# Optimization experiments

Measured on AMD Instinct MI355X. Metric: run time of the kernel, lower is better.

The kernel has to match this reference:

```python
import jax, jax.numpy as jnp
import numpy as np

N = 100000       # nodes
E = 3200000      # directed edges (before self-loops)
F_IN = 256       # num_node_features
HID = 8          # hidden per head (conv1)
HEADS = 8        # conv1 heads
C_OUT = 1        # conv2 out channels / heads=1


def setup_inputs() -> dict:
    key = jax.random.key(0)
    ks = jax.random.split(key, 10)
    s = 0.1
    return {
        "x": jax.random.normal(ks[0], (N, F_IN), jnp.float32),
        "edge_index": jax.random.randint(ks[1], (2, E), 0, N, dtype=jnp.int32),
        "W1": jax.random.normal(ks[2], (F_IN, HEADS * HID), jnp.float32) * s,
        "att_src1": jax.random.normal(ks[3], (HEADS, HID), jnp.float32) * s,
        "att_dst1": jax.random.normal(ks[4], (HEADS, HID), jnp.float32) * s,
        "b1": jnp.zeros((HEADS * HID,), jnp.float32),
        "W2": jax.random.normal(ks[5], (HEADS * HID, C_OUT), jnp.float32) * s,
        "att_src2": jax.random.normal(ks[6], (1, C_OUT), jnp.float32) * s,
        "att_dst2": jax.random.normal(ks[7], (1, C_OUT), jnp.float32) * s,
        "b2": jnp.zeros((C_OUT,), jnp.float32),
    }


def gat_conv(x, W, att_src, att_dst, bias, src, dst, heads, out_ch, concat):
    # PyG GATConv (eval mode): h = x @ W per head; alpha over incoming edges of dst.
    h = (x @ W).reshape(-1, heads, out_ch)                 # [N, H, C]
    a_s = jnp.einsum('nhc,hc->nh', h, att_src)             # source term
    a_d = jnp.einsum('nhc,hc->nh', h, att_dst)             # target term
    e = jax.nn.leaky_relu(a_s[src] + a_d[dst], 0.2)        # [Etot, H]
    # segment softmax over edges grouped by target node
    m = jax.ops.segment_max(e, dst, num_segments=N)
    ex = jnp.exp(e - m[dst])
    denom = jax.ops.segment_sum(ex, dst, num_segments=N)
    alpha = ex / (denom[dst] + 1e-16)                      # [Etot, H]
    out = jax.ops.segment_sum(h[src] * alpha[..., None], dst, num_segments=N)
    out = out.reshape(-1, heads * out_ch) if concat else out.mean(axis=1)
    return out + bias


def reference(x, edge_index, W1, att_src1, att_dst1, b1, W2, att_src2, att_dst2, b2):
    # add self-loops (GATConv default add_self_loops=True)
    loop = jnp.arange(N, dtype=edge_index.dtype)
    src = jnp.concatenate([edge_index[0], loop])
    dst = jnp.concatenate([edge_index[1], loop])
    # dropout layers are identity in eval mode
    h = gat_conv(x, W1, att_src1, att_dst1, b1, src, dst, HEADS, HID, True)
    h = jax.nn.elu(h)
    out = gat_conv(h, W2, att_src2, att_dst2, b2, src, dst, 1, C_OUT, False)
    return jax.nn.sigmoid(out)
```

## Files before the change

kernel.cpp:

```cpp
#include <hip/hip_runtime.h>
#include <math.h>

#define FIN 256
#define C1  64
#define NH  8
#define HID 8
#define MAXBUK 512
#define CAPLOG 14
#define SC_CHUNK 8192
#define EPT (SC_CHUNK / 512)

typedef unsigned short ushort_t;
typedef unsigned int uint_t;
typedef __attribute__((ext_vector_type(8))) short short8;
typedef __attribute__((ext_vector_type(4))) float f32x4;

__device__ __forceinline__ ushort_t f2bf(float f) {
    uint_t u = __float_as_uint(f);
    u += 0x7fffu + ((u >> 16) & 1u);
    return (ushort_t)(u >> 16);
}
__device__ __forceinline__ uint_t packbf2(float lo, float hi) {
    return (uint_t)f2bf(lo) | ((uint_t)f2bf(hi) << 16);
}
__device__ __forceinline__ float bf_lo(uint_t w) { return __uint_as_float(w << 16); }
__device__ __forceinline__ float bf_hi(uint_t w) { return __uint_as_float(w & 0xffff0000u); }

__global__ void k_prep(const float* __restrict__ W, ushort_t* __restrict__ Wtg,
                       int* __restrict__ bkt_cnt) {
    int tid = blockIdx.x * 256 + threadIdx.x;
    if (tid < MAXBUK) bkt_cnt[tid] = 0;
    int c = tid >> 8;
    int k = tid & 255;
    Wtg[c * 256 + k] = f2bf(W[k * C1 + c]);
}

__global__ __launch_bounds__(512) void k_bscatter(const int* __restrict__ ei, int E, int N,
                                                  int NBUK, int* __restrict__ bkt_cnt,
                                                  uint_t* __restrict__ ebuf) {
    __shared__ int hist[MAXBUK];
    __shared__ int loff[MAXBUK];
    __shared__ int delta[MAXBUK];
    __shared__ int ssum[MAXBUK];
    __shared__ uint_t vals[SC_CHUNK];
    __shared__ ushort_t buks[SC_CHUNK];

    const int t = threadIdx.x;
    hist[t] = 0;
    __syncthreads();

    const int Etot = E + N;
    const int base0 = blockIdx.x * SC_CHUNK;
    const int lim = min(base0 + SC_CHUNK, Etot);
    const int cnt = lim - base0;

    uint_t myval[EPT];
    int myb[EPT];
#pragma unroll
    for (int i = 0; i < EPT; ++i) {
        int e = base0 + t + i * 512;
        if (e < lim) {
            int s, d;
            if (e < E) { s = ei[e]; d = ei[E + e]; } else { s = e - E; d = s; }
            myval[i] = ((uint_t)s << 8) | (uint_t)(d & 255);
            myb[i] = d >> 8;
            atomicAdd(&hist[myb[i]], 1);
        } else myb[i] = -1;
    }
    __syncthreads();

    int v = hist[t];
    ssum[t] = v;
    __syncthreads();
    for (int o = 1; o < 512; o <<= 1) {
        int add = (t >= o) ? ssum[t - o] : 0;
        __syncthreads();
        ssum[t] += add;
        __syncthreads();
    }
    loff[t] = ssum[t] - v;
    __syncthreads();

    if (t < NBUK) {
        int c = hist[t];
        if (c) delta[t] = (t << CAPLOG) + atomicAdd(&bkt_cnt[t], c) - loff[t];
    }
    __syncthreads();

#pragma unroll
    for (int i = 0; i < EPT; ++i) {
        if (myb[i] >= 0) {
            int pos = atomicAdd(&loff[myb[i]], 1);
            vals[pos] = myval[i];
            buks[pos] = (ushort_t)myb[i];
        }
    }
    __syncthreads();

    for (int i = t; i < cnt; i += 512)
        ebuf[delta[buks[i]] + i] = vals[i];
}

__global__ __launch_bounds__(512) void k_bucket_csr(const uint_t* __restrict__ ebuf,
                                                    const int* __restrict__ bkt_cnt, int N,
                                                    int* __restrict__ deg, int* __restrict__ off,
                                                    int* __restrict__ csr) {
    __shared__ int degw[8 * 256];
    __shared__ int scan[256];
    __shared__ int curl[256];
    int b = blockIdx.x;
    int t = threadIdx.x;
    int wv = t >> 6;
    int beg = b << CAPLOG;
    int end = beg + bkt_cnt[b];
    for (int i = t; i < 8 * 256; i += 512) degw[i] = 0;
    __syncthreads();
    for (int j = beg + t; j < end; j += 512) {
        uint_t v = ebuf[j];
        atomicAdd(&degw[(wv << 8) + (v & 255u)], 1);
    }
    __syncthreads();
    int v = 0;
    if (t < 256) {
#pragma unroll
        for (int w = 0; w < 8; ++w) v += degw[(w << 8) + t];
        scan[t] = v;
    }
    __syncthreads();
    for (int o = 1; o < 256; o <<= 1) {
        int a = (t < 256 && t >= o) ? scan[t - o] : 0;
        __syncthreads();
        if (t < 256) scan[t] += a;
        __syncthreads();
    }
    if (t < 256) {
        int gpos = beg + scan[t] - v;
        int node = (b << 8) + t;
        if (node < N) { off[node] = gpos; deg[node] = v; }
        curl[t] = gpos;
    }
    __syncthreads();
    for (int j = beg + t; j < end; j += 512) {
        uint_t p = ebuf[j];
        int pos = atomicAdd(&curl[p & 255u], 1);
        csr[pos] = (int)(p >> 8);
    }
}

__global__ __launch_bounds__(256) void k_gemm1(
    const float* __restrict__ x, const ushort_t* __restrict__ Wtg,
    const float* __restrict__ att_s, const float* __restrict__ att_d,
    ushort_t* __restrict__ h1b, ushort_t* __restrict__ as1b, float* __restrict__ ad1, int N)
{
    const int t = threadIdx.x;
    const int wv = t >> 6, l = t & 63;
    const int l15 = l & 15, q = l >> 4;
    const int node = blockIdx.x * 64 + wv * 16 + l15;
    const bool ok = node < N;
    const float* xr = x + (size_t)(ok ? node : N - 1) * FIN;

    f32x4 acc[4];
#pragma unroll
    for (int ct = 0; ct < 4; ++ct) acc[ct] = (f32x4){0.f, 0.f, 0.f, 0.f};

    for (int kk = 0; kk < 8; ++kk) {
        const int kof = kk * 32 + q * 8;
        short8 af[4];
#pragma unroll
        for (int ct = 0; ct < 4; ++ct)
            af[ct] = *reinterpret_cast<const short8*>(&Wtg[(ct * 16 + l15) * 256 + kof]);
        const float4* xp = reinterpret_cast<const float4*>(xr + kof);
        float4 v0 = xp[0], v1 = xp[1];
        union { short8 s; uint_t u[4]; } bu;
        bu.u[0] = packbf2(v0.x, v0.y);
        bu.u[1] = packbf2(v0.z, v0.w);
        bu.u[2] = packbf2(v1.x, v1.y);
        bu.u[3] = packbf2(v1.z, v1.w);
#pragma unroll
        for (int ct = 0; ct < 4; ++ct)
            acc[ct] = __builtin_amdgcn_mfma_f32_16x16x32_bf16(af[ct], bu.s, acc[ct], 0, 0, 0);
    }

    float4 ats[4], atd4[4];
#pragma unroll
    for (int ct = 0; ct < 4; ++ct) {
        ats[ct]  = *reinterpret_cast<const float4*>(&att_s[ct * 16 + q * 4]);
        atd4[ct] = *reinterpret_cast<const float4*>(&att_d[ct * 16 + q * 4]);
    }
    const int hb = q >> 1;

    float asp[8], adp[8];
#pragma unroll
    for (int h = 0; h < 8; ++h) { asp[h] = 0.f; adp[h] = 0.f; }
#pragma unroll
    for (int ct = 0; ct < 4; ++ct) {
        f32x4 a = acc[ct];
        if (ok) {
            uint2 hv;
            hv.x = packbf2(a[0], a[1]);
            hv.y = packbf2(a[2], a[3]);
            *reinterpret_cast<uint2*>(&h1b[(size_t)node * C1 + ct * 16 + q * 4]) = hv;
        }
        int h = ct * 2 + hb;
        asp[h] = a[0] * ats[ct].x + a[1] * ats[ct].y + a[2] * ats[ct].z + a[3] * ats[ct].w;
        adp[h] = a[0] * atd4[ct].x + a[1] * atd4[ct].y + a[2] * atd4[ct].z + a[3] * atd4[ct].w;
    }
#pragma unroll
    for (int o = 16; o <= 32; o <<= 1) {
#pragma unroll
        for (int h = 0; h < 8; ++h) {
            asp[h] += __shfl_xor(asp[h], o, 64);
            adp[h] += __shfl_xor(adp[h], o, 64);
        }
    }
    if (q == 0 && ok) {
        uint4 aw;
        aw.x = packbf2(asp[0], asp[1]);
        aw.y = packbf2(asp[2], asp[3]);
        aw.z = packbf2(asp[4], asp[5]);
        aw.w = packbf2(asp[6], asp[7]);
        *reinterpret_cast<uint4*>(&as1b[(size_t)node * NH]) = aw;
        *reinterpret_cast<float4*>(&ad1[(size_t)node * NH]) =
            make_float4(adp[0], adp[1], adp[2], adp[3]);
        *reinterpret_cast<float4*>(&ad1[(size_t)node * NH + 4]) =
            make_float4(adp[4], adp[5], adp[6], adp[7]);
    }
}

__global__ __launch_bounds__(256) void k_agg1(
    const int* __restrict__ csr, const int* __restrict__ off, const int* __restrict__ deg,
    const ushort_t* __restrict__ as1b, const float* __restrict__ ad1,
    const ushort_t* __restrict__ h1b,
    const float* __restrict__ b1, const float* __restrict__ W2,
    float* __restrict__ h2, int N)
{
    int idx = blockIdx.x * 256 + threadIdx.x;
    int n = idx >> 4;
    if (n >= N) return;
    int sub  = threadIdx.x & 15;
    int hp   = sub & 3;
    int slot = sub >> 2;

    int beg = off[n];
    int end = beg + deg[n];

    float adv0 = ad1[(size_t)n * NH + 2 * hp];
    float adv1 = ad1[(size_t)n * NH + 2 * hp + 1];
    float den0 = 0.f, den1 = 0.f;
    float acc[16];
#pragma unroll
    for (int k = 0; k < 16; ++k) acc[k] = 0.f;

    for (int base = beg; base < end; base += 4) {
        int j = base + slot;
        int jj = j < end ? j : end - 1;
        int s = csr[jj];
        uint_t a2 = *reinterpret_cast<const uint_t*>(&as1b[(size_t)s * NH + 2 * hp]);
        float t0 = bf_lo(a2) + adv0;
        float t1 = bf_hi(a2) + adv1;
        t0 = fmaxf(t0, 0.2f * t0);
        t1 = fmaxf(t1, 0.2f * t1);
        bool live = j < end;
        float ex0 = live ? __expf(t0) : 0.f;
        float ex1 = live ? __expf(t1) : 0.f;
        den0 += ex0; den1 += ex1;
        const uint4* hbp = reinterpret_cast<const uint4*>(&h1b[(size_t)s * C1 + hp * 16]);
        uint4 u0 = hbp[0], u1 = hbp[1];
        acc[0]  = fmaf(ex0, bf_lo(u0.x), acc[0]);
        acc[1]  = fmaf(ex0, bf_hi(u0.x), acc[1]);
        acc[2]  = fmaf(ex0, bf_lo(u0.y), acc[2]);
        acc[3]  = fmaf(ex0, bf_hi(u0.y), acc[3]);
        acc[4]  = fmaf(ex0, bf_lo(u0.z), acc[4]);
        acc[5]  = fmaf(ex0, bf_hi(u0.z), acc[5]);
        acc[6]  = fmaf(ex0, bf_lo(u0.w), acc[6]);
        acc[7]  = fmaf(ex0, bf_hi(u0.w), acc[7]);
        acc[8]  = fmaf(ex1, bf_lo(u1.x), acc[8]);
        acc[9]  = fmaf(ex1, bf_hi(u1.x), acc[9]);
        acc[10] = fmaf(ex1, bf_lo(u1.y), acc[10]);
        acc[11] = fmaf(ex1, bf_hi(u1.y), acc[11]);
        acc[12] = fmaf(ex1, bf_lo(u1.z), acc[12]);
        acc[13] = fmaf(ex1, bf_hi(u1.z), acc[13]);
        acc[14] = fmaf(ex1, bf_lo(u1.w), acc[14]);
        acc[15] = fmaf(ex1, bf_hi(u1.w), acc[15]);
    }

#pragma unroll
    for (int o = 4; o <= 8; o <<= 1) {
        den0 += __shfl_xor(den0, o, 64);
        den1 += __shfl_xor(den1, o, 64);
#pragma unroll
        for (int k = 0; k < 16; ++k) acc[k] += __shfl_xor(acc[k], o, 64);
    }

    float inv0 = 1.f / (den0 + 1e-16f);
    float inv1 = 1.f / (den1 + 1e-16f);
    const float4* bp = reinterpret_cast<const float4*>(&b1[hp * 16]);
    const float4* wp = reinterpret_cast<const float4*>(&W2[hp * 16]);
    float bb[16], ww[16];
#pragma unroll
    for (int i = 0; i < 4; ++i) {
        float4 b4 = bp[i], w4 = wp[i];
        bb[4 * i] = b4.x; bb[4 * i + 1] = b4.y; bb[4 * i + 2] = b4.z; bb[4 * i + 3] = b4.w;
        ww[4 * i] = w4.x; ww[4 * i + 1] = w4.y; ww[4 * i + 2] = w4.z; ww[4 * i + 3] = w4.w;
    }
    float p = 0.f;
#pragma unroll
    for (int k = 0; k < 16; ++k) {
        float inv = (k < 8) ? inv0 : inv1;
        float v = acc[k] * inv + bb[k];
        v = v > 0.f ? v : (__expf(v) - 1.f);
        p = fmaf(v, ww[k], p);
    }
#pragma unroll
    for (int o = 1; o <= 2; o <<= 1) p += __shfl_xor(p, o, 64);
    if (sub == 0) h2[n] = p;
}

__global__ __launch_bounds__(256) void k_agg2(
    const int* __restrict__ csr, const int* __restrict__ off, const int* __restrict__ deg,
    const float* __restrict__ h2,
    const float* __restrict__ ats2, const float* __restrict__ atd2,
    const float* __restrict__ b2, float* __restrict__ out, int N)
{
    int idx = blockIdx.x * 256 + threadIdx.x;
    int n = idx >> 4;
    int l16 = threadIdx.x & 15;
    if (n >= N) return;
    int beg = off[n];
    int end = beg + deg[n];
    float a_s = ats2[0], a_d = atd2[0];
    float adv = h2[n] * a_d;
    float den = 0.f, num = 0.f;
    for (int j = beg + l16; j < end; j += 16) {
        float hs = h2[csr[j]];
        float t = fmaf(hs, a_s, adv);
        t = fmaxf(t, 0.2f * t);
        float ex = __expf(t);
        den += ex;
        num = fmaf(ex, hs, num);
    }
#pragma unroll
    for (int o = 1; o <= 8; o <<= 1) {
        den += __shfl_xor(den, o, 64);
        num += __shfl_xor(num, o, 64);
    }
    if (l16 == 0) {
        float t = num / (den + 1e-16f) + b2[0];
        out[n] = 1.f / (1.f + __expf(-t));
    }
}

extern "C" void kernel_launch(void* const* d_in, const int* in_sizes, int n_in,
                              void* d_out, int out_size, void* d_ws, size_t ws_size,
                              hipStream_t stream)
{
    const float* x    = (const float*)d_in[0];
    const int*   ei   = (const int*)d_in[1];
    const float* W1   = (const float*)d_in[2];
    const float* ats1 = (const float*)d_in[3];
    const float* atd1 = (const float*)d_in[4];
    const float* b1   = (const float*)d_in[5];
    const float* W2   = (const float*)d_in[6];
    const float* ats2 = (const float*)d_in[7];
    const float* atd2 = (const float*)d_in[8];
    const float* b2   = (const float*)d_in[9];
    float* out = (float*)d_out;

    const int N = out_size;
    const int E = in_sizes[1] / 2;
    const int Etot = E + N;
    const int NBUK = (N + 255) >> 8;
    const size_t capElems = (size_t)NBUK << CAPLOG;

    char* base = (char*)d_ws;
    uint_t* ebuf = (uint_t*)base;
    ushort_t* h1b  = (ushort_t*)base;
    ushort_t* as1b = h1b + (size_t)N * C1;
    float* ad1 = (float*)(as1b + (size_t)N * NH);
    float* h2  = ad1 + (size_t)N * NH;
    size_t featBytes = (size_t)N * (C1 * 2 + NH * 2 + NH * 4 + 4);
    size_t unionBytes = capElems * sizeof(uint_t);
    if (featBytes > unionBytes) unionBytes = featBytes;
    unionBytes = (unionBytes + 255) & ~(size_t)255;
    int* deg     = (int*)(base + unionBytes);
    int* off     = deg + N;
    int* bkt_cnt = off + N;
    int* csr     = bkt_cnt + MAXBUK;
    ushort_t* wtg = (ushort_t*)(csr + capElems);

    k_prep<<<64, 256, 0, stream>>>(W1, wtg, bkt_cnt);
    k_bscatter<<<(Etot + SC_CHUNK - 1) / SC_CHUNK, 512, 0, stream>>>(ei, E, N, NBUK, bkt_cnt, ebuf);
    k_bucket_csr<<<NBUK, 512, 0, stream>>>(ebuf, bkt_cnt, N, deg, off, csr);

    k_gemm1<<<(N + 63) / 64, 256, 0, stream>>>(x, wtg, ats1, atd1, h1b, as1b, ad1, N);
    k_agg1<<<(N * 16 + 255) / 256, 256, 0, stream>>>(csr, off, deg, as1b, ad1, h1b, b1, W2, h2, N);
    k_agg2<<<(N * 16 + 255) / 256, 256, 0, stream>>>(csr, off, deg, h2, ats2, atd2, b2, out, N);
}
```

Baseline: 331.2 us.

## Sort CSR neighbors by source slice and sweep slices in lockstep for locality

The CSR build now sub-sorts each destination's neighbor list into 8 source-index slices and records per-node per-slice counts packed into bytes. The layer-1 aggregation is rewritten so each block processes 64 nodes slice by slice, keeping partial sums in shared memory. All threads then gather from the same source range at once, which should improve L2 hit rates on h1b/as1b. The cost is a larger shared-memory scan in the CSR build and shared-memory state traffic across slices. The byte-packed counts overflow if any node has more than 255 neighbors in one slice.

Result: slower. 358.6 us (+8.3%).

```diff
diff --git a/kernel.cpp b/kernel.cpp
--- a/kernel.cpp
+++ b/kernel.cpp
@@ -9,6 +9,8 @@
 #define CAPLOG 14
 #define SC_CHUNK 8192
 #define EPT (SC_CHUNK / 512)
+#define NSLICE 8
+#define SLDIV 12500u
 
 typedef unsigned short ushort_t;
 typedef unsigned int uint_t;
@@ -104,46 +106,62 @@
 __global__ __launch_bounds__(512) void k_bucket_csr(const uint_t* __restrict__ ebuf,
                                                     const int* __restrict__ bkt_cnt, int N,
                                                     int* __restrict__ deg, int* __restrict__ off,
-                                                    int* __restrict__ csr) {
-    __shared__ int degw[8 * 256];
-    __shared__ int scan[256];
-    __shared__ int curl[256];
+                                                    int* __restrict__ csr,
+                                                    uint2* __restrict__ pcnt) {
+    __shared__ int hist[256 * NSLICE];
+    __shared__ int ssum[512];
     int b = blockIdx.x;
     int t = threadIdx.x;
-    int wv = t >> 6;
     int beg = b << CAPLOG;
     int end = beg + bkt_cnt[b];
-    for (int i = t; i < 8 * 256; i += 512) degw[i] = 0;
+    for (int i = t; i < 256 * NSLICE; i += 512) hist[i] = 0;
     __syncthreads();
     for (int j = beg + t; j < end; j += 512) {
         uint_t v = ebuf[j];
-        atomicAdd(&degw[(wv << 8) + (v & 255u)], 1);
-    }
-    __syncthreads();
-    int v = 0;
+        int key = ((v & 255u) << 3) | ((v >> 8) / SLDIV);
+        atomicAdd(&hist[key], 1);
+    }
+    __syncthreads();
     if (t < 256) {
-#pragma unroll
-        for (int w = 0; w < 8; ++w) v += degw[(w << 8) + t];
-        scan[t] = v;
-    }
-    __syncthreads();
-    for (int o = 1; o < 256; o <<= 1) {
-        int a = (t < 256 && t >= o) ? scan[t - o] : 0;
+        int node = (b << 8) + t;
+        int c[8]; int s = 0;
+#pragma unroll
+        for (int i = 0; i < 8; ++i) { c[i] = hist[(t << 3) | i]; s += c[i]; }
+        if (node < N) {
+            deg[node] = s;
+            uint2 pc;
+            pc.x = (uint_t)c[0] | ((uint_t)c[1] << 8) | ((uint_t)c[2] << 16) | ((uint_t)c[3] << 24);
+            pc.y = (uint_t)c[4] | ((uint_t)c[5] << 8) | ((uint_t)c[6] << 16) | ((uint_t)c[7] << 24);
+            pcnt[node] = pc;
+        }
+    }
+    int c0 = hist[4 * t], c1 = hist[4 * t + 1], c2 = hist[4 * t + 2], c3 = hist[4 * t + 3];
+    int s4 = c0 + c1 + c2 + c3;
+    __syncthreads();
+    ssum[t] = s4;
+    __syncthreads();
+    for (int o = 1; o < 512; o <<= 1) {
+        int add = (t >= o) ? ssum[t - o] : 0;
         __syncthreads();
-        if (t < 256) scan[t] += a;
+        ssum[t] += add;
         __syncthreads();
     }
+    int base = beg + ssum[t] - s4;
+    hist[4 * t]     = base;
+    hist[4 * t + 1] = base + c0;
+    hist[4 * t + 2] = base + c0 + c1;
+    hist[4 * t + 3] = base + c0 + c1 + c2;
+    __syncthreads();
     if (t < 256) {
-        int gpos = beg + scan[t] - v;
         int node = (b << 8) + t;
-        if (node < N) { off[node] = gpos; deg[node] = v; }
-        curl[t] = gpos;
+        if (node < N) off[node] = hist[t << 3];
     }
     __syncthreads();
     for (int j = beg + t; j < end; j += 512) {
-        uint_t p = ebuf[j];
-        int pos = atomicAdd(&curl[p & 255u], 1);
-        csr[pos] = (int)(p >> 8);
+        uint_t v = ebuf[j];
+        int key = ((v & 255u) << 3) | ((v >> 8) / SLDIV);
+        int pos = atomicAdd(&hist[key], 1);
+        csr[pos] = (int)(v >> 8);
     }
 }
 
@@ -227,93 +245,94 @@
     }
 }
 
-__global__ __launch_bounds__(256) void k_agg1(
-    const int* __restrict__ csr, const int* __restrict__ off, const int* __restrict__ deg,
+__global__ __launch_bounds__(256, 7) void k_agg1(
+    const int* __restrict__ csr, const int* __restrict__ off, const uint2* __restrict__ pcnt,
     const ushort_t* __restrict__ as1b, const float* __restrict__ ad1,
     const ushort_t* __restrict__ h1b,
     const float* __restrict__ b1, const float* __restrict__ W2,
     float* __restrict__ h2, int N)
 {
-    int idx = blockIdx.x * 256 + threadIdx.x;
-    int n = idx >> 4;
-    if (n >= N) return;
-    int sub  = threadIdx.x & 15;
-    int hp   = sub & 3;
-    int slot = sub >> 2;
-
-    int beg = off[n];
-    int end = beg + deg[n];
-
-    float adv0 = ad1[(size_t)n * NH + 2 * hp];
-    float adv1 = ad1[(size_t)n * NH + 2 * hp + 1];
-    float den0 = 0.f, den1 = 0.f;
-    float acc[16];
-#pragma unroll
-    for (int k = 0; k < 16; ++k) acc[k] = 0.f;
-
-    for (int base = beg; base < end; base += 4) {
-        int j = base + slot;
-        int jj = j < end ? j : end - 1;
-        int s = csr[jj];
-        uint_t a2 = *reinterpret_cast<const uint_t*>(&as1b[(size_t)s * NH + 2 * hp]);
-        float t0 = bf_lo(a2) + adv0;
-        float t1 = bf_hi(a2) + adv1;
-        t0 = fmaxf(t0, 0.2f * t0);
-        t1 = fmaxf(t1, 0.2f * t1);
-        bool live = j < end;
-        float ex0 = live ? __expf(t0) : 0.f;
-        float ex1 = live ? __expf(t1) : 0.f;
-        den0 += ex0; den1 += ex1;
-        const uint4* hbp = reinterpret_cast<const uint4*>(&h1b[(size_t)s * C1 + hp * 16]);
-        uint4 u0 = hbp[0], u1 = hbp[1];
-        acc[0]  = fmaf(ex0, bf_lo(u0.x), acc[0]);
-        acc[1]  = fmaf(ex0, bf_hi(u0.x), acc[1]);
-        acc[2]  = fmaf(ex0, bf_lo(u0.y), acc[2]);
-        acc[3]  = fmaf(ex0, bf_hi(u0.y), acc[3]);
-        acc[4]  = fmaf(ex0, bf_lo(u0.z), acc[4]);
-        acc[5]  = fmaf(ex0, bf_hi(u0.z), acc[5]);
-        acc[6]  = fmaf(ex0, bf_lo(u0.w), acc[6]);
-        acc[7]  = fmaf(ex0, bf_hi(u0.w), acc[7]);
-        acc[8]  = fmaf(ex1, bf_lo(u1.x), acc[8]);
-        acc[9]  = fmaf(ex1, bf_hi(u1.x), acc[9]);
-        acc[10] = fmaf(ex1, bf_lo(u1.y), acc[10]);
-        acc[11] = fmaf(ex1, bf_hi(u1.y), acc[11]);
-        acc[12] = fmaf(ex1, bf_lo(u1.z), acc[12]);
-        acc[13] = fmaf(ex1, bf_hi(u1.z), acc[13]);
-        acc[14] = fmaf(ex1, bf_lo(u1.w), acc[14]);
-        acc[15] = fmaf(ex1, bf_hi(u1.w), acc[15]);
-    }
-
-#pragma unroll
-    for (int o = 4; o <= 8; o <<= 1) {
-        den0 += __shfl_xor(den0, o, 64);
-        den1 += __shfl_xor(den1, o, 64);
-#pragma unroll
-        for (int k = 0; k < 16; ++k) acc[k] += __shfl_xor(acc[k], o, 64);
-    }
-
-    float inv0 = 1.f / (den0 + 1e-16f);
-    float inv1 = 1.f / (den1 + 1e-16f);
-    const float4* bp = reinterpret_cast<const float4*>(&b1[hp * 16]);
-    const float4* wp = reinterpret_cast<const float4*>(&W2[hp * 16]);
-    float bb[16], ww[16];
-#pragma unroll
-    for (int i = 0; i < 4; ++i) {
-        float4 b4 = bp[i], w4 = wp[i];
-        bb[4 * i] = b4.x; bb[4 * i + 1] = b4.y; bb[4 * i + 2] = b4.z; bb[4 * i + 3] = b4.w;
-        ww[4 * i] = w4.x; ww[4 * i + 1] = w4.y; ww[4 * i + 2] = w4.z; ww[4 * i + 3] = w4.w;
-    }
-    float p = 0.f;
-#pragma unroll
-    for (int k = 0; k < 16; ++k) {
-        float inv = (k < 8) ? inv0 : inv1;
-        float v = acc[k] * inv + bb[k];
-        v = v > 0.f ? v : (__expf(v) - 1.f);
-        p = fmaf(v, ww[k], p);
-    }
-#pragma unroll
-    for (int o = 1; o <= 2; o <<= 1) p += __shfl_xor(p, o, 64);
-    if (sub == 0) h2[n] = p;
+    __shared__ float st[2][256][9];
+    __shared__ int curp[2][32];
+    const int t = threadIdx.x;
+    const int row = t >> 3, f = t & 7;
+    const int n0 = blockIdx.x * 64;
+
+#pragma unroll
+    for (int g = 0; g < 2; ++g) {
+#pragma unroll
+        for (int k = 0; k < 9; ++k) st[g][t][k] = 0.f;
+        if (f == 0) {
+            int n = n0 + g * 32 + row;
+            curp[g][row] = (n < N) ? off[n] : 0;
+        }
+    }
+
+    for (int p = 0; p < NSLICE; ++p) {
+#pragma unroll
+        for (int g = 0; g < 2; ++g) {
+            const int n = n0 + g * 32 + row;
+            const bool ok = n < N;
+            int cnt = 0, cur = 0;
+            float adv = 0.f;
+            if (ok) {
+                uint2 pc = pcnt[n];
+                uint_t w = (p < 4) ? pc.x : pc.y;
+                cnt = (w >> ((p & 3) * 8)) & 255u;
+                cur = curp[g][row];
+                adv = ad1[(size_t)n * NH + f];
+            }
+            float a0 = st[g][t][0], a1 = st[g][t][1], a2 = st[g][t][2], a3 = st[g][t][3];
+            float a4 = st[g][t][4], a5 = st[g][t][5], a6 = st[g][t][6], a7 = st[g][t][7];
+            float den = st[g][t][8];
+            for (int i = 0; i < cnt; ++i) {
+                int s = csr[cur + i];
+                float asv = __uint_as_float((uint_t)as1b[(size_t)s * NH + f] << 16);
+                float tt = asv + adv;
+                tt = fmaxf(tt, 0.2f * tt);
+                float ex = __expf(tt);
+                den += ex;
+                uint4 hv = *reinterpret_cast<const uint4*>(&h1b[(size_t)s * C1 + f * 8]);
+                a0 = fmaf(ex, bf_lo(hv.x), a0);
+                a1 = fmaf(ex, bf_hi(hv.x), a1);
+                a2 = fmaf(ex, bf_lo(hv.y), a2);
+                a3 = fmaf(ex, bf_hi(hv.y), a3);
+                a4 = fmaf(ex, bf_lo(hv.z), a4);
+                a5 = fmaf(ex, bf_hi(hv.z), a5);
+                a6 = fmaf(ex, bf_lo(hv.w), a6);
+                a7 = fmaf(ex, bf_hi(hv.w), a7);
+            }
+            st[g][t][0] = a0; st[g][t][1] = a1; st[g][t][2] = a2; st[g][t][3] = a3;
+            st[g][t][4] = a4; st[g][t][5] = a5; st[g][t][6] = a6; st[g][t][7] = a7;
+            st[g][t][8] = den;
+            if (f == 0 && ok) curp[g][row] = cur + cnt;
+        }
+    }
+
+#pragma unroll
+    for (int g = 0; g < 2; ++g) {
+        const int n = n0 + g * 32 + row;
+        if (n >= N) continue;
+        float den = st[g][t][8];
+        float inv = 1.f / (den + 1e-16f);
+        float4 ba = *reinterpret_cast<const float4*>(&b1[f * 8]);
+        float4 bb = *reinterpret_cast<const float4*>(&b1[f * 8 + 4]);
+        float4 wa = *reinterpret_cast<const float4*>(&W2[f * 8]);
+        float4 wb = *reinterpret_cast<const float4*>(&W2[f * 8 + 4]);
+        float bv[8] = {ba.x, ba.y, ba.z, ba.w, bb.x, bb.y, bb.z, bb.w};
+        float wv[8] = {wa.x, wa.y, wa.z, wa.w, wb.x, wb.y, wb.z, wb.w};
+        float ps = 0.f;
+#pragma unroll
+        for (int k = 0; k < 8; ++k) {
+            float v = st[g][t][k] * inv + bv[k];
+            v = v > 0.f ? v : (__expf(v) - 1.f);
+            ps = fmaf(v, wv[k], ps);
+        }
+        ps += __shfl_xor(ps, 1, 64);
+        ps += __shfl_xor(ps, 2, 64);
+        ps += __shfl_xor(ps, 4, 64);
+        if (f == 0) h2[n] = ps;
+    }
 }
 
 __global__ __launch_bounds__(256) void k_agg2(
@@ -386,13 +405,14 @@
     int* off     = deg + N;
     int* bkt_cnt = off + N;
     int* csr     = bkt_cnt + MAXBUK;
-    ushort_t* wtg = (ushort_t*)(csr + capElems);
+    uint2* pcnt  = (uint2*)(csr + capElems);
+    ushort_t* wtg = (ushort_t*)(pcnt + N);
 
     k_prep<<<64, 256, 0, stream>>>(W1, wtg, bkt_cnt);
     k_bscatter<<<(Etot + SC_CHUNK - 1) / SC_CHUNK, 512, 0, stream>>>(ei, E, N, NBUK, bkt_cnt, ebuf);
-    k_bucket_csr<<<NBUK, 512, 0, stream>>>(ebuf, bkt_cnt, N, deg, off, csr);
+    k_bucket_csr<<<NBUK, 512, 0, stream>>>(ebuf, bkt_cnt, N, deg, off, csr, pcnt);
 
     k_gemm1<<<(N + 63) / 64, 256, 0, stream>>>(x, wtg, ats1, atd1, h1b, as1b, ad1, N);
-    k_agg1<<<(N * 16 + 255) / 256, 256, 0, stream>>>(csr, off, deg, as1b, ad1, h1b, b1, W2, h2, N);
+    k_agg1<<<(N + 63) / 64, 256, 0, stream>>>(csr, off, pcnt, as1b, ad1, h1b, b1, W2, h2, N);
     k_agg2<<<(N * 16 + 255) / 256, 256, 0, stream>>>(csr, off, deg, h2, ats2, atd2, b2, out, N);
 }
```

## Slice CSR neighbors by source range and use persistent grid for layer-1 aggregation

Applied to the files above, without the earlier changes.

The CSR build now keys each edge by destination and by one of eight source-id slices, so every node's neighbor list is sorted into source-range groups. Per-slice counts are packed into a uint2 per node. k_agg1 becomes a grid-stride persistent kernel that walks the slices in order, so concurrent warps tend to gather h1b rows from similar address ranges and get better L2 locality. The cost is a larger scan in the CSR build, a division per edge, and a per-slice inner loop with more loop overhead and possible lane imbalance. Packed counts assume fewer than 256 edges per node per slice.

Result: slower. 363.7 us (+9.8%).

```diff
diff --git a/kernel.cpp b/kernel.cpp
--- a/kernel.cpp
+++ b/kernel.cpp
@@ -9,6 +9,9 @@
 #define CAPLOG 14
 #define SC_CHUNK 8192
 #define EPT (SC_CHUNK / 512)
+#define NSLICE 8
+#define SLDIV 12500u
+#define AGG_GRID 2048
 
 typedef unsigned short ushort_t;
 typedef unsigned int uint_t;
@@ -104,46 +107,62 @@
 __global__ __launch_bounds__(512) void k_bucket_csr(const uint_t* __restrict__ ebuf,
                                                     const int* __restrict__ bkt_cnt, int N,
                                                     int* __restrict__ deg, int* __restrict__ off,
-                                                    int* __restrict__ csr) {
-    __shared__ int degw[8 * 256];
-    __shared__ int scan[256];
-    __shared__ int curl[256];
+                                                    int* __restrict__ csr,
+                                                    uint2* __restrict__ pcnt) {
+    __shared__ int hist[256 * NSLICE];
+    __shared__ int ssum[512];
     int b = blockIdx.x;
     int t = threadIdx.x;
-    int wv = t >> 6;
     int beg = b << CAPLOG;
     int end = beg + bkt_cnt[b];
-    for (int i = t; i < 8 * 256; i += 512) degw[i] = 0;
+    for (int i = t; i < 256 * NSLICE; i += 512) hist[i] = 0;
     __syncthreads();
     for (int j = beg + t; j < end; j += 512) {
         uint_t v = ebuf[j];
-        atomicAdd(&degw[(wv << 8) + (v & 255u)], 1);
-    }
-    __syncthreads();
-    int v = 0;
+        int key = ((v & 255u) << 3) | ((v >> 8) / SLDIV);
+        atomicAdd(&hist[key], 1);
+    }
+    __syncthreads();
     if (t < 256) {
-#pragma unroll
-        for (int w = 0; w < 8; ++w) v += degw[(w << 8) + t];
-        scan[t] = v;
-    }
-    __syncthreads();
-    for (int o = 1; o < 256; o <<= 1) {
-        int a = (t < 256 && t >= o) ? scan[t - o] : 0;
+        int node = (b << 8) + t;
+        int c[8]; int s = 0;
+#pragma unroll
+        for (int i = 0; i < 8; ++i) { c[i] = hist[(t << 3) | i]; s += c[i]; }
+        if (node < N) {
+            deg[node] = s;
+            uint2 pc;
+            pc.x = (uint_t)c[0] | ((uint_t)c[1] << 8) | ((uint_t)c[2] << 16) | ((uint_t)c[3] << 24);
+            pc.y = (uint_t)c[4] | ((uint_t)c[5] << 8) | ((uint_t)c[6] << 16) | ((uint_t)c[7] << 24);
+            pcnt[node] = pc;
+        }
+    }
+    int c0 = hist[4 * t], c1 = hist[4 * t + 1], c2 = hist[4 * t + 2], c3 = hist[4 * t + 3];
+    int s4 = c0 + c1 + c2 + c3;
+    __syncthreads();
+    ssum[t] = s4;
+    __syncthreads();
+    for (int o = 1; o < 512; o <<= 1) {
+        int add = (t >= o) ? ssum[t - o] : 0;
         __syncthreads();
-        if (t < 256) scan[t] += a;
+        ssum[t] += add;
         __syncthreads();
     }
+    int base = beg + ssum[t] - s4;
+    hist[4 * t]     = base;
+    hist[4 * t + 1] = base + c0;
+    hist[4 * t + 2] = base + c0 + c1;
+    hist[4 * t + 3] = base + c0 + c1 + c2;
+    __syncthreads();
     if (t < 256) {
-        int gpos = beg + scan[t] - v;
         int node = (b << 8) + t;
-        if (node < N) { off[node] = gpos; deg[node] = v; }
-        curl[t] = gpos;
+        if (node < N) off[node] = hist[t << 3];
     }
     __syncthreads();
     for (int j = beg + t; j < end; j += 512) {
-        uint_t p = ebuf[j];
-        int pos = atomicAdd(&curl[p & 255u], 1);
-        csr[pos] = (int)(p >> 8);
+        uint_t v = ebuf[j];
+        int key = ((v & 255u) << 3) | ((v >> 8) / SLDIV);
+        int pos = atomicAdd(&hist[key], 1);
+        csr[pos] = (int)(v >> 8);
     }
 }
 
@@ -227,73 +246,18 @@
     }
 }
 
-__global__ __launch_bounds__(256) void k_agg1(
-    const int* __restrict__ csr, const int* __restrict__ off, const int* __restrict__ deg,
+__global__ __launch_bounds__(256, 8) void k_agg1(
+    const int* __restrict__ csr, const int* __restrict__ off, const uint2* __restrict__ pcnt,
     const ushort_t* __restrict__ as1b, const float* __restrict__ ad1,
     const ushort_t* __restrict__ h1b,
     const float* __restrict__ b1, const float* __restrict__ W2,
     float* __restrict__ h2, int N)
 {
-    int idx = blockIdx.x * 256 + threadIdx.x;
-    int n = idx >> 4;
-    if (n >= N) return;
-    int sub  = threadIdx.x & 15;
-    int hp   = sub & 3;
-    int slot = sub >> 2;
-
-    int beg = off[n];
-    int end = beg + deg[n];
-
-    float adv0 = ad1[(size_t)n * NH + 2 * hp];
-    float adv1 = ad1[(size_t)n * NH + 2 * hp + 1];
-    float den0 = 0.f, den1 = 0.f;
-    float acc[16];
-#pragma unroll
-    for (int k = 0; k < 16; ++k) acc[k] = 0.f;
-
-    for (int base = beg; base < end; base += 4) {
-        int j = base + slot;
-        int jj = j < end ? j : end - 1;
-        int s = csr[jj];
-        uint_t a2 = *reinterpret_cast<const uint_t*>(&as1b[(size_t)s * NH + 2 * hp]);
-        float t0 = bf_lo(a2) + adv0;
-        float t1 = bf_hi(a2) + adv1;
-        t0 = fmaxf(t0, 0.2f * t0);
-        t1 = fmaxf(t1, 0.2f * t1);
-        bool live = j < end;
-        float ex0 = live ? __expf(t0) : 0.f;
-        float ex1 = live ? __expf(t1) : 0.f;
-        den0 += ex0; den1 += ex1;
-        const uint4* hbp = reinterpret_cast<const uint4*>(&h1b[(size_t)s * C1 + hp * 16]);
-        uint4 u0 = hbp[0], u1 = hbp[1];
-        acc[0]  = fmaf(ex0, bf_lo(u0.x), acc[0]);
-        acc[1]  = fmaf(ex0, bf_hi(u0.x), acc[1]);
-        acc[2]  = fmaf(ex0, bf_lo(u0.y), acc[2]);
-        acc[3]  = fmaf(ex0, bf_hi(u0.y), acc[3]);
-        acc[4]  = fmaf(ex0, bf_lo(u0.z), acc[4]);
-        acc[5]  = fmaf(ex0, bf_hi(u0.z), acc[5]);
-        acc[6]  = fmaf(ex0, bf_lo(u0.w), acc[6]);
-        acc[7]  = fmaf(ex0, bf_hi(u0.w), acc[7]);
-        acc[8]  = fmaf(ex1, bf_lo(u1.x), acc[8]);
-        acc[9]  = fmaf(ex1, bf_hi(u1.x), acc[9]);
-        acc[10] = fmaf(ex1, bf_lo(u1.y), acc[10]);
-        acc[11] = fmaf(ex1, bf_hi(u1.y), acc[11]);
-        acc[12] = fmaf(ex1, bf_lo(u1.z), acc[12]);
-        acc[13] = fmaf(ex1, bf_hi(u1.z), acc[13]);
-        acc[14] = fmaf(ex1, bf_lo(u1.w), acc[14]);
-        acc[15] = fmaf(ex1, bf_hi(u1.w), acc[15]);
-    }
-
-#pragma unroll
-    for (int o = 4; o <= 8; o <<= 1) {
-        den0 += __shfl_xor(den0, o, 64);
-        den1 += __shfl_xor(den1, o, 64);
-#pragma unroll
-        for (int k = 0; k < 16; ++k) acc[k] += __shfl_xor(acc[k], o, 64);
-    }
-
-    float inv0 = 1.f / (den0 + 1e-16f);
-    float inv1 = 1.f / (den1 + 1e-16f);
+    const int sub  = threadIdx.x & 15;
+    const int hp   = sub & 3;
+    const int slot = sub >> 2;
+    const int rowb = threadIdx.x >> 4;
+
     const float4* bp = reinterpret_cast<const float4*>(&b1[hp * 16]);
     const float4* wp = reinterpret_cast<const float4*>(&W2[hp * 16]);
     float bb[16], ww[16];
@@ -303,17 +267,78 @@
         bb[4 * i] = b4.x; bb[4 * i + 1] = b4.y; bb[4 * i + 2] = b4.z; bb[4 * i + 3] = b4.w;
         ww[4 * i] = w4.x; ww[4 * i + 1] = w4.y; ww[4 * i + 2] = w4.z; ww[4 * i + 3] = w4.w;
     }
-    float p = 0.f;
-#pragma unroll
-    for (int k = 0; k < 16; ++k) {
-        float inv = (k < 8) ? inv0 : inv1;
-        float v = acc[k] * inv + bb[k];
-        v = v > 0.f ? v : (__expf(v) - 1.f);
-        p = fmaf(v, ww[k], p);
-    }
-#pragma unroll
-    for (int o = 1; o <= 2; o <<= 1) p += __shfl_xor(p, o, 64);
-    if (sub == 0) h2[n] = p;
+
+    for (int tile = blockIdx.x; tile * 16 < N; tile += gridDim.x) {
+        const int n = tile * 16 + rowb;
+        const bool okn = n < N;
+        const int nn = okn ? n : N - 1;
+
+        int cur = off[nn];
+        const uint2 pc = pcnt[nn];
+        const float adv0 = ad1[(size_t)nn * NH + 2 * hp];
+        const float adv1 = ad1[(size_t)nn * NH + 2 * hp + 1];
+        float den0 = 0.f, den1 = 0.f;
+        float acc[16];
+#pragma unroll
+        for (int k = 0; k < 16; ++k) acc[k] = 0.f;
+
+        for (int p = 0; p < NSLICE; ++p) {
+            const uint_t w = (p < 4) ? pc.x : pc.y;
+            const int cnt = (w >> ((p & 3) * 8)) & 255u;
+            for (int i = slot; i < cnt; i += 4) {
+                int s = csr[cur + i];
+                uint_t a2 = *reinterpret_cast<const uint_t*>(&as1b[(size_t)s * NH + 2 * hp]);
+                float t0 = bf_lo(a2) + adv0;
+                float t1 = bf_hi(a2) + adv1;
+                t0 = fmaxf(t0, 0.2f * t0);
+                t1 = fmaxf(t1, 0.2f * t1);
+                float ex0 = __expf(t0);
+                float ex1 = __expf(t1);
+                den0 += ex0; den1 += ex1;
+                const uint4* hbp = reinterpret_cast<const uint4*>(&h1b[(size_t)s * C1 + hp * 16]);
+                uint4 u0 = hbp[0], u1 = hbp[1];
+                acc[0]  = fmaf(ex0, bf_lo(u0.x), acc[0]);
+                acc[1]  = fmaf(ex0, bf_hi(u0.x), acc[1]);
+                acc[2]  = fmaf(ex0, bf_lo(u0.y), acc[2]);
+                acc[3]  = fmaf(ex0, bf_hi(u0.y), acc[3]);
+                acc[4]  = fmaf(ex0, bf_lo(u0.z), acc[4]);
+                acc[5]  = fmaf(ex0, bf_hi(u0.z), acc[5]);
+                acc[6]  = fmaf(ex0, bf_lo(u0.w), acc[6]);
+                acc[7]  = fmaf(ex0, bf_hi(u0.w), acc[7]);
+                acc[8]  = fmaf(ex1, bf_lo(u1.x), acc[8]);
+                acc[9]  = fmaf(ex1, bf_hi(u1.x), acc[9]);
+                acc[10] = fmaf(ex1, bf_lo(u1.y), acc[10]);
+                acc[11] = fmaf(ex1, bf_hi(u1.y), acc[11]);
+                acc[12] = fmaf(ex1, bf_lo(u1.z), acc[12]);
+                acc[13] = fmaf(ex1, bf_hi(u1.z), acc[13]);
+                acc[14] = fmaf(ex1, bf_lo(u1.w), acc[14]);
+                acc[15] = fmaf(ex1, bf_hi(u1.w), acc[15]);
+            }
+            cur += cnt;
+        }
+
+#pragma unroll
+        for (int o = 4; o <= 8; o <<= 1) {
+            den0 += __shfl_xor(den0, o, 64);
+            den1 += __shfl_xor(den1, o, 64);
+#pragma unroll
+            for (int k = 0; k < 16; ++k) acc[k] += __shfl_xor(acc[k], o, 64);
+        }
+
+        float inv0 = 1.f / (den0 + 1e-16f);
+        float inv1 = 1.f / (den1 + 1e-16f);
+        float p2 = 0.f;
+#pragma unroll
+        for (int k = 0; k < 16; ++k) {
+            float inv = (k < 8) ? inv0 : inv1;
+            float v = acc[k] * inv + bb[k];
+            v = v > 0.f ? v : (__expf(v) - 1.f);
+            p2 = fmaf(v, ww[k], p2);
+        }
+#pragma unroll
+        for (int o = 1; o <= 2; o <<= 1) p2 += __shfl_xor(p2, o, 64);
+        if (sub == 0 && okn) h2[n] = p2;
+    }
 }
 
 __global__ __launch_bounds__(256) void k_agg2(
@@ -386,13 +411,14 @@
     int* off     = deg + N;
     int* bkt_cnt = off + N;
     int* csr     = bkt_cnt + MAXBUK;
-    ushort_t* wtg = (ushort_t*)(csr + capElems);
+    uint2* pcnt  = (uint2*)(csr + capElems);
+    ushort_t* wtg = (ushort_t*)(pcnt + N);
 
     k_prep<<<64, 256, 0, stream>>>(W1, wtg, bkt_cnt);
     k_bscatter<<<(Etot + SC_CHUNK - 1) / SC_CHUNK, 512, 0, stream>>>(ei, E, N, NBUK, bkt_cnt, ebuf);
-    k_bucket_csr<<<NBUK, 512, 0, stream>>>(ebuf, bkt_cnt, N, deg, off, csr);
+    k_bucket_csr<<<NBUK, 512, 0, stream>>>(ebuf, bkt_cnt, N, deg, off, csr, pcnt);
 
     k_gemm1<<<(N + 63) / 64, 256, 0, stream>>>(x, wtg, ats1, atd1, h1b, as1b, ad1, N);
-    k_agg1<<<(N * 16 + 255) / 256, 256, 0, stream>>>(csr, off, deg, as1b, ad1, h1b, b1, W2, h2, N);
+    k_agg1<<<AGG_GRID, 256, 0, stream>>>(csr, off, pcnt, as1b, ad1, h1b, b1, W2, h2, N);
     k_agg2<<<(N * 16 + 255) / 256, 256, 0, stream>>>(csr, off, deg, h2, ats2, atd2, b2, out, N);
 }
```
